# Optimization experiments

Hardware: AMD Instinct MI355X
Metric: run time of the kernel (lower is better)

Reference implementation:

```python
import jax, jax.numpy as jnp
import numpy as np

IN_F = 4096
OUT_F = 4096
BLOCK = 32            # oft_block_size
NBLK = IN_F // BLOCK  # 128 rotation blocks
GROUP = 8             # AQLM group size
NCB = 1               # num codebooks
CB_SIZE = 65536       # 2**16 codes


def setup_inputs() -> dict:
    key = jax.random.key(0)
    k = jax.random.split(key, 6)
    x = jax.random.normal(k[0], (4, 4096, IN_F), dtype=jnp.float32)
    # unconstrained OFT parameter; skew-symmetrized inside the Cayley transform
    oft_r = jax.random.normal(k[1], (NBLK, BLOCK, BLOCK), dtype=jnp.float32) * 0.01
    codes = jax.random.randint(k[2], (OUT_F, IN_F // GROUP, NCB), 0, CB_SIZE, dtype=jnp.int32)
    codebooks = jax.random.normal(k[3], (NCB, CB_SIZE, GROUP), dtype=jnp.float32) * 0.02
    scales = jax.random.uniform(k[4], (OUT_F, 1), dtype=jnp.float32, minval=0.5, maxval=1.5)
    bias = jax.random.normal(k[5], (OUT_F,), dtype=jnp.float32) * 0.01
    return {"x": x, "oft_r": oft_r, "codes": codes, "codebooks": codebooks,
            "scales": scales, "bias": bias}


def _cayley(oft_r):
    # skew-symmetrize then exact Cayley transform: Q = (I + S)(I - S)^{-1}, orthogonal
    S = 0.5 * (oft_r - jnp.swapaxes(oft_r, -1, -2))  # [NBLK, B, B]
    I = jnp.eye(BLOCK, dtype=oft_r.dtype)
    A = I - S
    Bm = I + S
    # Q = Bm @ inv(A)  <=>  Q^T = solve(A^T, Bm^T)
    Qt = jnp.linalg.solve(jnp.swapaxes(A, -1, -2), jnp.swapaxes(Bm, -1, -2))
    return jnp.swapaxes(Qt, -1, -2)  # [NBLK, B, B]


def _dequant_weight(codes, codebooks, scales):
    # codes: [O, G, K] -> gather per-codebook vectors and sum -> [O, G, gs]
    K = codebooks.shape[0]
    gathered = codebooks[jnp.arange(K)[None, None, :], codes]  # [O, G, K, gs]
    w = gathered.sum(axis=2).reshape(codes.shape[0], -1)       # [O, IN_F]
    return w * scales                                          # row-wise scale


def reference(x, oft_r, codes, codebooks, scales, bias):
    expected_dtype = x.dtype
    x = x.astype(oft_r.dtype)  # cast to adapter dtype
    # block-diagonal orthogonal rotation of the input features
    Q = _cayley(oft_r)  # [NBLK, B, B]
    B_, S_, D_ = x.shape
    xb = x.reshape(B_, S_, NBLK, BLOCK)
    xr = jnp.einsum('bsnj,njk->bsnk', xb, Q).reshape(B_, S_, D_)
    # AQLM dequantized linear
    W = _dequant_weight(codes, codebooks, scales)  # [OUT_F, IN_F]
    out = jnp.einsum('bsd,od->bso', xr, W) + bias
    return out.astype(expected_dtype)
```

## Files before the change

kernel.cpp:

```cpp
#include <hip/hip_runtime.h>
#include <cstdint>
#include <cstddef>

#define IN_F 4096
#define OUT_F 4096
#define MTOT 16384
#define NBLKS 128

typedef __bf16 bf16x8 __attribute__((ext_vector_type(8)));
typedef float f32x4 __attribute__((ext_vector_type(4)));
typedef const __attribute__((address_space(1))) void* gas_cvp;
typedef __attribute__((address_space(3))) void* las_vp;

__device__ __forceinline__ unsigned short f2bf(float f) {
  unsigned u = __builtin_bit_cast(unsigned, f);
  u += 0x7fffu + ((u >> 16) & 1u);
  return (unsigned short)(u >> 16);
}

__global__ void cayley_kernel(const float* __restrict__ R, float* __restrict__ Q) {
  __shared__ float M[32][66];
  const int n = blockIdx.x;
  const int t = threadIdx.x;
  const int i = t >> 5, j = t & 31;
  const float* Rb = R + n * 1024;
  const float s = 0.5f * (Rb[i * 32 + j] - Rb[j * 32 + i]);
  M[i][j]      = (i == j ? 1.0f : 0.0f) - s;
  M[i][32 + j] = (i == j ? 1.0f : 0.0f) + s;
  __syncthreads();
  for (int k = 0; k < 32; ++k) {
    const float pivinv = 1.0f / M[k][k];
    const float fik = M[i][k];
    const float mk1 = M[k][j] * pivinv;
    const float mk2 = M[k][32 + j] * pivinv;
    __syncthreads();
    if (i == k) {
      M[i][j] = mk1;
      M[i][32 + j] = mk2;
    } else {
      M[i][j]      -= fik * mk1;
      M[i][32 + j] -= fik * mk2;
    }
    __syncthreads();
  }
  Q[n * 1024 + i * 32 + j] = M[i][32 + j];
}

__global__ void dequant_kernel(const int* __restrict__ codes,
                               const float* __restrict__ cb,
                               const float* __restrict__ scales,
                               unsigned short* __restrict__ W) {
  const int idx = blockIdx.x * 256 + threadIdx.x;
  const int o = idx >> 9;
  const int code = codes[idx];
  const float s = scales[o];
  const float4* cp = (const float4*)(cb + (size_t)code * 8);
  const float4 a = cp[0], b = cp[1];
  uint4 p;
  p.x = (unsigned)f2bf(a.x * s) | ((unsigned)f2bf(a.y * s) << 16);
  p.y = (unsigned)f2bf(a.z * s) | ((unsigned)f2bf(a.w * s) << 16);
  p.z = (unsigned)f2bf(b.x * s) | ((unsigned)f2bf(b.y * s) << 16);
  p.w = (unsigned)f2bf(b.z * s) | ((unsigned)f2bf(b.w * s) << 16);
  ((uint4*)W)[idx] = p;
}

__global__ __launch_bounds__(256) void rotate_kernel(
    const float* __restrict__ x, const float* __restrict__ Q,
    unsigned short* __restrict__ xr) {
  __shared__ float Qs[1024];
  const int n = blockIdx.y;
  const int t = threadIdx.x;
#pragma unroll
  for (int i = 0; i < 4; ++i) Qs[t + i * 256] = Q[n * 1024 + t + i * 256];
  __syncthreads();
  const long m = (long)blockIdx.x * 256 + t;
  const float4* xp = (const float4*)(x + m * IN_F + n * 32);
  float4 xv[8];
#pragma unroll
  for (int j4 = 0; j4 < 8; ++j4) xv[j4] = xp[j4];
  float4 acc[8] = {};
  const float* xs = (const float*)xv;
#pragma unroll
  for (int j = 0; j < 32; ++j) {
    const float xj = xs[j];
#pragma unroll
    for (int c4 = 0; c4 < 8; ++c4) {
      const float4 q = ((const float4*)Qs)[j * 8 + c4];
      acc[c4].x += xj * q.x;
      acc[c4].y += xj * q.y;
      acc[c4].z += xj * q.z;
      acc[c4].w += xj * q.w;
    }
  }
  uint4* op = (uint4*)(xr + m * IN_F + n * 32);
#pragma unroll
  for (int g = 0; g < 4; ++g) {
    const float4 a = acc[2 * g], b = acc[2 * g + 1];
    uint4 p;
    p.x = (unsigned)f2bf(a.x) | ((unsigned)f2bf(a.y) << 16);
    p.y = (unsigned)f2bf(a.z) | ((unsigned)f2bf(a.w) << 16);
    p.z = (unsigned)f2bf(b.x) | ((unsigned)f2bf(b.y) << 16);
    p.w = (unsigned)f2bf(b.z) | ((unsigned)f2bf(b.w) << 16);
    op[g] = p;
  }
}

#define BM 128
#define BN 128
#define BK 64

__global__ __launch_bounds__(256) void gemm_kernel(
    const __bf16* __restrict__ A, const __bf16* __restrict__ B,
    const float* __restrict__ bias, float* __restrict__ C,
    const int M, const int N, const int K) {
  __shared__ __attribute__((aligned(16))) __bf16 As[BM * BK];
  __shared__ __attribute__((aligned(16))) __bf16 Bs[BN * BK];
  const int t = threadIdx.x;
  const int l = t & 63;
  const int w = t >> 6;
  const int wm = w >> 1, wn = w & 1;
  const int lr = l & 15;
  const int kg = l >> 4;
  const long m0 = (long)blockIdx.y * BM;
  const long n0 = (long)blockIdx.x * BN;

  int off[4];
#pragma unroll
  for (int q = 0; q < 4; ++q) {
    const int s = (w * 4 + q) * 64 + l;
    const int row = s >> 3;
    const int csrc = (s & 7) ^ (row & 7);
    off[q] = row * K + csrc * 8;
  }

  f32x4 acc[4][4] = {};

  for (int k0 = 0; k0 < K; k0 += BK) {
    const __bf16* Ab = A + m0 * K + k0;
    const __bf16* Bb = B + n0 * K + k0;
#pragma unroll
    for (int q = 0; q < 4; ++q) {
      __builtin_amdgcn_global_load_lds((gas_cvp)(Ab + off[q]),
                                       (las_vp)(As + (w * 4 + q) * 512), 16, 0, 0);
      __builtin_amdgcn_global_load_lds((gas_cvp)(Bb + off[q]),
                                       (las_vp)(Bs + (w * 4 + q) * 512), 16, 0, 0);
    }
    __syncthreads();

#pragma unroll
    for (int kk = 0; kk < 2; ++kk) {
      bf16x8 af[4], bf[4];
      const int cc = kk * 4 + kg;
      const int jl = cc ^ (lr & 7);
#pragma unroll
      for (int i = 0; i < 4; ++i) {
        const int r = wm * 64 + i * 16 + lr;
        af[i] = *(const bf16x8*)(As + r * BK + jl * 8);
      }
#pragma unroll
      for (int j = 0; j < 4; ++j) {
        const int r = wn * 64 + j * 16 + lr;
        bf[j] = *(const bf16x8*)(Bs + r * BK + jl * 8);
      }
#pragma unroll
      for (int i = 0; i < 4; ++i)
#pragma unroll
        for (int j = 0; j < 4; ++j)
          acc[i][j] = __builtin_amdgcn_mfma_f32_16x16x32_bf16(af[i], bf[j], acc[i][j], 0, 0, 0);
    }
    __syncthreads();
  }

#pragma unroll
  for (int j = 0; j < 4; ++j) {
    const long gn = n0 + wn * 64 + j * 16 + lr;
    const float bv = bias[gn];
#pragma unroll
    for (int i = 0; i < 4; ++i) {
#pragma unroll
      for (int r = 0; r < 4; ++r) {
        const long gm = m0 + wm * 64 + i * 16 + kg * 4 + r;
        C[gm * (long)N + gn] = acc[i][j][r] + bv;
      }
    }
  }
}

extern "C" void kernel_launch(void* const* d_in, const int* in_sizes, int n_in,
                              void* d_out, int out_size, void* d_ws, size_t ws_size,
                              hipStream_t stream) {
  const float* x         = (const float*)d_in[0];
  const float* oft_r     = (const float*)d_in[1];
  const int*   codes     = (const int*)d_in[2];
  const float* codebooks = (const float*)d_in[3];
  const float* scales    = (const float*)d_in[4];
  const float* bias      = (const float*)d_in[5];
  float* out = (float*)d_out;

  char* ws = (char*)d_ws;
  float* Q = (float*)ws;
  unsigned short* XR = (unsigned short*)(ws + (1 << 19));
  unsigned short* W  = (unsigned short*)(ws + (1 << 19) + (size_t)MTOT * IN_F * 2);

  cayley_kernel<<<NBLKS, 1024, 0, stream>>>(oft_r, Q);
  dequant_kernel<<<(OUT_F * (IN_F / 8)) / 256, 256, 0, stream>>>(codes, codebooks, scales, W);
  rotate_kernel<<<dim3(MTOT / 256, NBLKS), 256, 0, stream>>>(x, Q, XR);
  gemm_kernel<<<dim3(OUT_F / BN, MTOT / BM), 256, 0, stream>>>(
      (const __bf16*)XR, (const __bf16*)W, bias, out, MTOT, OUT_F, IN_F);
}
```

Baseline: 1.279 ms.

## Rewrite GEMM with 256x256 tiles and a 4-stage async LDS pipeline

Replaces the single-buffered 128x128 bf16 MFMA GEMM with 256x256 tiles, 512 threads and a 4-deep ring of LDS buffers. Tiles are prefetched via global_load_lds three steps ahead, with vmcnt waits in place of full barriers around each load. It also adds an XCD-aware block-index swizzle, raises MFMA issue priority with s_setprio, and uses a different LDS XOR swizzle. The goal is to hide global-memory latency and improve operand reuse and L2 locality. In exchange it uses much more LDS and registers (acc[8][4] per thread), which may limit occupancy.

```diff
diff --git a/kernel.cpp b/kernel.cpp
--- a/kernel.cpp
+++ b/kernel.cpp
@@ -105,82 +105,126 @@
   }
 }
 
-#define BM 128
-#define BN 128
-#define BK 64
-
-__global__ __launch_bounds__(256) void gemm_kernel(
+#define G_BM 256
+#define G_BN 256
+#define G_BK 32
+#define G_KT 128
+
+__global__ __launch_bounds__(512, 2) void gemm_kernel(
     const __bf16* __restrict__ A, const __bf16* __restrict__ B,
-    const float* __restrict__ bias, float* __restrict__ C,
-    const int M, const int N, const int K) {
-  __shared__ __attribute__((aligned(16))) __bf16 As[BM * BK];
-  __shared__ __attribute__((aligned(16))) __bf16 Bs[BN * BK];
+    const float* __restrict__ bias, float* __restrict__ C) {
+  __shared__ __attribute__((aligned(16))) __bf16 As[4][G_BM * G_BK];
+  __shared__ __attribute__((aligned(16))) __bf16 Bs[4][G_BN * G_BK];
+
   const int t = threadIdx.x;
   const int l = t & 63;
   const int w = t >> 6;
-  const int wm = w >> 1, wn = w & 1;
+  const int wm = w >> 2;
+  const int wn = w & 3;
   const int lr = l & 15;
   const int kg = l >> 4;
-  const long m0 = (long)blockIdx.y * BM;
-  const long n0 = (long)blockIdx.x * BN;
-
-  int off[4];
-#pragma unroll
-  for (int q = 0; q < 4; ++q) {
-    const int s = (w * 4 + q) * 64 + l;
-    const int row = s >> 3;
-    const int csrc = (s & 7) ^ (row & 7);
-    off[q] = row * K + csrc * 8;
-  }
-
-  f32x4 acc[4][4] = {};
-
-  for (int k0 = 0; k0 < K; k0 += BK) {
-    const __bf16* Ab = A + m0 * K + k0;
-    const __bf16* Bb = B + n0 * K + k0;
-#pragma unroll
-    for (int q = 0; q < 4; ++q) {
-      __builtin_amdgcn_global_load_lds((gas_cvp)(Ab + off[q]),
-                                       (las_vp)(As + (w * 4 + q) * 512), 16, 0, 0);
-      __builtin_amdgcn_global_load_lds((gas_cvp)(Bb + off[q]),
-                                       (las_vp)(Bs + (w * 4 + q) * 512), 16, 0, 0);
-    }
-    __syncthreads();
-
-#pragma unroll
-    for (int kk = 0; kk < 2; ++kk) {
-      bf16x8 af[4], bf[4];
-      const int cc = kk * 4 + kg;
-      const int jl = cc ^ (lr & 7);
-#pragma unroll
-      for (int i = 0; i < 4; ++i) {
-        const int r = wm * 64 + i * 16 + lr;
-        af[i] = *(const bf16x8*)(As + r * BK + jl * 8);
-      }
-#pragma unroll
-      for (int j = 0; j < 4; ++j) {
-        const int r = wn * 64 + j * 16 + lr;
-        bf[j] = *(const bf16x8*)(Bs + r * BK + jl * 8);
-      }
-#pragma unroll
-      for (int i = 0; i < 4; ++i)
-#pragma unroll
-        for (int j = 0; j < 4; ++j)
-          acc[i][j] = __builtin_amdgcn_mfma_f32_16x16x32_bf16(af[i], bf[j], acc[i][j], 0, 0, 0);
-    }
-    __syncthreads();
-  }
+
+  const int bid = blockIdx.x;
+  const int wg = (bid & 7) * 128 + (bid >> 3);
+  const int bx = wg & 15;
+  const int by = wg >> 4;
+  const long m0 = (long)by * G_BM;
+  const long n0 = (long)bx * G_BN;
+
+  const __bf16* Abase = A + m0 * IN_F;
+  const __bf16* Bbase = B + n0 * IN_F;
+
+  int goff[2], soff[2];
+#pragma unroll
+  for (int q = 0; q < 2; ++q) {
+    const int ri = w * 2 + q;
+    const int s = ri * 64 + l;
+    const int row = s >> 2;
+    const int jj = s & 3;
+    const int csrc = jj ^ ((row >> 1) & 3);
+    goff[q] = row * IN_F + csrc * 8;
+    soff[q] = ri * 512;
+  }
+
+  const int chunk = kg ^ ((lr >> 1) & 3);
+  int aoff[8], boff[4];
+#pragma unroll
+  for (int i = 0; i < 8; ++i) aoff[i] = (wm * 128 + i * 16 + lr) * G_BK + chunk * 8;
+#pragma unroll
+  for (int j = 0; j < 4; ++j) boff[j] = (wn * 64 + j * 16 + lr) * G_BK + chunk * 8;
+
+  f32x4 acc[8][4] = {};
+
+#define STAGE(buf, kt) do {                                                   \
+    const __bf16* Ak_ = Abase + (kt) * G_BK;                                  \
+    const __bf16* Bk_ = Bbase + (kt) * G_BK;                                  \
+    _Pragma("unroll")                                                         \
+    for (int q_ = 0; q_ < 2; ++q_) {                                          \
+      __builtin_amdgcn_global_load_lds((gas_cvp)(Ak_ + goff[q_]),             \
+                                       (las_vp)(&As[(buf)][0] + soff[q_]), 16, 0, 0); \
+      __builtin_amdgcn_global_load_lds((gas_cvp)(Bk_ + goff[q_]),             \
+                                       (las_vp)(&Bs[(buf)][0] + soff[q_]), 16, 0, 0); \
+    }                                                                         \
+  } while (0)
+
+#define COMPUTE(buf) do {                                                     \
+    bf16x8 af_[8], bf_[4];                                                    \
+    _Pragma("unroll")                                                         \
+    for (int i_ = 0; i_ < 8; ++i_)                                            \
+      af_[i_] = *(const bf16x8*)(&As[(buf)][0] + aoff[i_]);                   \
+    _Pragma("unroll")                                                         \
+    for (int j_ = 0; j_ < 4; ++j_)                                            \
+      bf_[j_] = *(const bf16x8*)(&Bs[(buf)][0] + boff[j_]);                   \
+    __builtin_amdgcn_s_setprio(1);                                            \
+    _Pragma("unroll")                                                         \
+    for (int i_ = 0; i_ < 8; ++i_)                                            \
+      _Pragma("unroll")                                                       \
+      for (int j_ = 0; j_ < 4; ++j_)                                          \
+        acc[i_][j_] = __builtin_amdgcn_mfma_f32_16x16x32_bf16(                \
+            af_[i_], bf_[j_], acc[i_][j_], 0, 0, 0);                          \
+    __builtin_amdgcn_s_setprio(0);                                            \
+  } while (0)
+
+#define TILE_SYNC(n) do {                                                     \
+    asm volatile("s_waitcnt vmcnt(" #n ")" ::: "memory");                     \
+    __builtin_amdgcn_s_barrier();                                             \
+    asm volatile("" ::: "memory");                                            \
+  } while (0)
+
+  STAGE(0, 0);
+  STAGE(1, 1);
+  STAGE(2, 2);
+  TILE_SYNC(8);
+
+#pragma unroll 4
+  for (int kt = 0; kt < G_KT - 4; ++kt) {
+    STAGE((kt + 3) & 3, kt + 3);
+    COMPUTE(kt & 3);
+    TILE_SYNC(8);
+  }
+  STAGE(3, 127);
+  COMPUTE(0);
+  TILE_SYNC(8);
+  COMPUTE(1);
+  TILE_SYNC(4);
+  COMPUTE(2);
+  TILE_SYNC(0);
+  COMPUTE(3);
+
+#undef STAGE
+#undef COMPUTE
+#undef TILE_SYNC
 
 #pragma unroll
   for (int j = 0; j < 4; ++j) {
     const long gn = n0 + wn * 64 + j * 16 + lr;
     const float bv = bias[gn];
 #pragma unroll
-    for (int i = 0; i < 4; ++i) {
+    for (int i = 0; i < 8; ++i) {
+      const long gm = m0 + wm * 128 + i * 16 + kg * 4;
 #pragma unroll
       for (int r = 0; r < 4; ++r) {
-        const long gm = m0 + wm * 64 + i * 16 + kg * 4 + r;
-        C[gm * (long)N + gn] = acc[i][j][r] + bv;
+        C[(gm + r) * (long)OUT_F + gn] = acc[i][j][r] + bv;
       }
     }
   }
@@ -205,6 +249,6 @@
   cayley_kernel<<<NBLKS, 1024, 0, stream>>>(oft_r, Q);
   dequant_kernel<<<(OUT_F * (IN_F / 8)) / 256, 256, 0, stream>>>(codes, codebooks, scales, W);
   rotate_kernel<<<dim3(MTOT / 256, NBLKS), 256, 0, stream>>>(x, Q, XR);
-  gemm_kernel<<<dim3(OUT_F / BN, MTOT / BM), 256, 0, stream>>>(
-      (const __bf16*)XR, (const __bf16*)W, bias, out, MTOT, OUT_F, IN_F);
-}
+  gemm_kernel<<<dim3((MTOT / G_BM) * (OUT_F / G_BN)), 512, 0, stream>>>(
+      (const __bf16*)XR, (const __bf16*)W, bias, out);
+}
```

After: 1.168 ms. 8.6% less time.
